# Kernel tuning notes

Hardware: AMD Instinct MI355X
Metric: run time of the kernel (lower is better)

The kernel has to match this reference:

```python
import jax, jax.numpy as jnp
import numpy as np

N, E, IN, H, OUT, L = 100000, 1600000, 128, 64, 64, 3


def setup_inputs() -> dict:
    key = jax.random.key(0)
    ks = jax.random.split(key, 20)
    g = lambda i, shape: jax.random.normal(ks[i], shape, dtype=jnp.float32) * 0.05
    # architecture mixture weights: softmax of log_alpha ~ N(1, 0.01)
    sm = lambda i, rows, n: jax.nn.softmax(1.0 + 0.01 * jax.random.normal(ks[i], (rows, n), dtype=jnp.float32), axis=-1)
    return dict(
        x=jax.random.normal(ks[0], (N, IN), dtype=jnp.float32),
        edge_index=jax.random.randint(ks[1], (2, E), 0, N, dtype=jnp.int32),
        W_pre=g(2, (IN, H)), b_pre=jnp.zeros((H,), jnp.float32),
        W_self=g(3, (L, H, H)), b_self=jnp.zeros((L, H), jnp.float32),
        W_nbr=g(4, (L, H, H)), b_nbr=jnp.zeros((L, H), jnp.float32),
        W_comb=g(5, (L, 2 * H, H)), b_comb=jnp.zeros((L, H), jnp.float32),
        W_lc=g(6, (L, 2 * H, H)), b_lc=jnp.zeros((L, H), jnp.float32),
        ln_g=jnp.ones((L, H), jnp.float32), ln_b=jnp.zeros((L, H), jnp.float32),
        prelu_w=jnp.full((L,), 0.25, jnp.float32),
        W_lagg=g(7, ((L + 1) * H, H)), b_lagg=jnp.zeros((H,), jnp.float32),
        W_ff1=g(8, (H, H)), b_ff1=jnp.zeros((H,), jnp.float32),
        W_ff2=g(9, (H, OUT)), b_ff2=jnp.zeros((OUT,), jnp.float32),
        Z_agg=sm(10, L, 3), Z_comb=sm(11, L, 2), Z_act=sm(12, L, 2),
        Z_lc=sm(13, L, 3), Z_lagg=sm(14, 1, 3),
    )


def _layernorm(x, g, b, eps=1e-5):
    mu = x.mean(-1, keepdims=True)
    var = ((x - mu) ** 2).mean(-1, keepdims=True)
    return (x - mu) / jnp.sqrt(var + eps) * g + b


def reference(x, edge_index, W_pre, b_pre, W_self, b_self, W_nbr, b_nbr,
              W_comb, b_comb, W_lc, b_lc, ln_g, ln_b, prelu_w,
              W_lagg, b_lagg, W_ff1, b_ff1, W_ff2, b_ff2,
              Z_agg, Z_comb, Z_act, Z_lc, Z_lagg):
    n = x.shape[0]
    src, tgt = edge_index[0], edge_index[1]
    cnt = jax.ops.segment_sum(jnp.ones((src.shape[0], 1), x.dtype), tgt, num_segments=n)
    x = x @ W_pre + b_pre                       # preprocess: [N, H]
    embs = [x]
    for i in range(L):
        x_self = x @ W_self[i] + b_self[i]
        x_nl = x @ W_nbr[i] + b_nbr[i]
        msg = x_nl[src]                         # gather messages [E, H]
        s = jax.ops.segment_sum(msg, tgt, num_segments=n)
        mean = s / jnp.maximum(cnt, 1.0)
        mx = jax.ops.segment_max(msg, tgt, num_segments=n)
        mx = jnp.where(cnt > 0, mx, 0.0)        # empty segments -> 0 (PyG convention)
        x_n = Z_agg[i, 0] * s + Z_agg[i, 1] * mean + Z_agg[i, 2] * mx
        # combine mixture: sum / concat+merge
        c_sum = x_self + x_n
        c_cat = jnp.concatenate([x_self, x_n], -1) @ W_comb[i] + b_comb[i]
        h = Z_comb[i, 0] * c_sum + Z_comb[i, 1] * c_cat
        # act mixture: relu / prelu
        h = Z_act[i, 0] * jax.nn.relu(h) + Z_act[i, 1] * jnp.where(h > 0, h, prelu_w[i] * h)
        h = _layernorm(h, ln_g[i], ln_b[i])
        embs.append(h)
        # layer_connect mixture: stack / skip_sum / skip_cat
        lc_cat = jnp.concatenate([embs[-2], embs[-1]], -1) @ W_lc[i] + b_lc[i]
        x = Z_lc[i, 0] * h + Z_lc[i, 1] * (h + embs[-2]) + Z_lc[i, 2] * lc_cat
    # layer_agg mixture: none / max_pooling / concat+merge over emb_list
    a_none = embs[-1]
    a_max = jnp.stack(embs, 0).max(0)
    a_cat = jnp.concatenate(embs, -1) @ W_lagg + b_lagg
    out = Z_lagg[0, 0] * a_none + Z_lagg[0, 1] * a_max + Z_lagg[0, 2] * a_cat
    # feed-forward head (node-level task, no global pooling)
    out = jax.nn.relu(out @ W_ff1 + b_ff1) @ W_ff2 + b_ff2
    return out
```

## Files before the change

### kernel.cpp

```cpp
#include <hip/hip_runtime.h>

typedef unsigned short u16;
typedef unsigned int u32;
using bfrag = __attribute__((ext_vector_type(8))) short;
using f4v   = __attribute__((ext_vector_type(4))) float;

#define DIV_UP(a,b) (((a)+(b)-1)/(b))
#define PTILE 4096
#define CHB 512
#define CHSH 9
#define NBKT 256
#define MFMA(a,b,c) __builtin_amdgcn_mfma_f32_16x16x32_bf16(a,b,c,0,0,0)

__device__ inline u16 f2bf(float f){
  union { float f; u32 u; } v; v.f = f;
  u32 u = v.u;
  return (u16)((u + 0x7fffu + ((u >> 16) & 1u)) >> 16);
}
__device__ inline float bf2f(u16 h){
  union { u32 u; float f; } v; v.u = ((u32)h) << 16;
  return v.f;
}
__device__ inline bfrag ldA(const u16* A, long r, int koff, int lane){
  return *reinterpret_cast<const bfrag*>(A + r*64 + koff + ((lane>>4)<<3));
}
__device__ inline bfrag ldW(const u16* Wf, int kb, int cb, int lane){
  return *reinterpret_cast<const bfrag*>(Wf + (((kb*4+cb)*64 + lane)<<3));
}

__device__ inline void xpose_store(u16* sT, int lane, const f4v (&acc)[4]){
  const int cl = lane & 15, g = lane >> 4;
#pragma unroll
  for (int j = 0; j < 4; ++j){
    const int lr = g*4 + j;
#pragma unroll
    for (int cb = 0; cb < 4; ++cb){
      const int colblk = cb*2 + (cl >> 3);
      const int gr = colblk ^ (lr & 7);
      sT[lr*64 + gr*8 + (cl & 7)] = f2bf(acc[cb][j]);
    }
  }
}
__device__ inline bfrag xpose_load(const u16* sT, int lane, int kb){
  const int row = lane & 15, colblk = kb*4 + (lane >> 4);
  const int gr = colblk ^ (row & 7);
  return *reinterpret_cast<const bfrag*>(sT + row*64 + gr*8);
}

__global__ void initBkt_k(int* __restrict__ bktCnt, int bstride){
  if (threadIdx.x < NBKT) bktCnt[threadIdx.x] = threadIdx.x * bstride;
}
__global__ void partition_k(const int* __restrict__ tgt, const int* __restrict__ src,
                            int E, int* __restrict__ bktCnt, int2* __restrict__ bkt){
  __shared__ int hist[NBKT], base[NBKT], pos[NBKT];
  const int t = threadIdx.x;
  hist[t] = 0;
  __syncthreads();
  const int e0 = blockIdx.x * PTILE;
  const int e1 = (e0 + PTILE < E) ? e0 + PTILE : E;
  for (int i = e0 + t; i < e1; i += NBKT)
    atomicAdd(&hist[tgt[i] >> CHSH], 1);
  __syncthreads();
  base[t] = (hist[t] > 0) ? atomicAdd(&bktCnt[t], hist[t]) : 0;
  pos[t] = 0;
  __syncthreads();
  for (int i = e0 + t; i < e1; i += NBKT){
    int tv = tgt[i], sv = src[i];
    int c = tv >> CHSH;
    int p = base[c] + atomicAdd(&pos[c], 1);
    bkt[p] = make_int2(tv, sv);
  }
}

__global__ __launch_bounds__(CHB) void sortChunk_k(const int2* __restrict__ bkt,
    const int* __restrict__ bktCnt, int bstride, int N,
    int* __restrict__ cnt, int* __restrict__ off, int* __restrict__ perm){
  __shared__ int hist[CHB], sbase[CHB];
  const int c = blockIdx.x, t = threadIdx.x;
  const int lo = c * CHB;
  const int s = c * bstride, e = bktCnt[c];
  hist[t] = 0;
  __syncthreads();
  for (int i = s + t; i < e; i += CHB)
    atomicAdd(&hist[bkt[i].x - lo], 1);
  __syncthreads();
  const int v = hist[t];
  for (int o = 1; o < CHB; o <<= 1){
    int add = (t >= o) ? hist[t - o] : 0;
    __syncthreads();
    hist[t] += add;
    __syncthreads();
  }
  const int excl = hist[t] - v;
  if (lo + t < N){ cnt[lo + t] = v; off[lo + t] = s + excl; }
  sbase[t] = s + excl;
  __syncthreads();
  hist[t] = 0;
  __syncthreads();
  for (int i = s + t; i < e; i += CHB){
    int2 ed = bkt[i];
    int r = ed.x - lo;
    int p = sbase[r] + atomicAdd(&hist[r], 1);
    perm[p] = ed.y;
  }
}

__global__ void matW_k(const float* __restrict__ W_self, const float* __restrict__ W_comb,
                       const float* __restrict__ b_self,
                       float* __restrict__ WsWct, float* __restrict__ bsWct){
  const int b = blockIdx.x;
  const int i = b / 65, r = b % 65;
  const int c = threadIdx.x;
  const float* Wc = W_comb + i*8192;
  float s = 0.f;
  if (r < 64){
    const float* a = W_self + i*4096 + r*64;
#pragma unroll 8
    for (int k = 0; k < 64; ++k) s += a[k] * Wc[k*64 + c];
    WsWct[i*4096 + r*64 + c] = s;
  } else {
    const float* a = b_self + i*64;
#pragma unroll 8
    for (int k = 0; k < 64; ++k) s += a[k] * Wc[k*64 + c];
    bsWct[i*64 + c] = s;
  }
}

__global__ void buildAll_k(const float* __restrict__ W_self, const float* __restrict__ W_comb,
    const float* __restrict__ b_self, const float* __restrict__ b_comb,
    const float* __restrict__ Z_comb, const float* __restrict__ WsWct,
    const float* __restrict__ bsWct,
    const float* __restrict__ W_lc, const float* __restrict__ b_lc,
    const float* __restrict__ Z_lc,
    const float* __restrict__ W_lagg, const float* __restrict__ b_lagg,
    const float* __restrict__ Z_lagg,
    float* __restrict__ W1eff, float* __restrict__ W2eff, float* __restrict__ beff,
    float* __restrict__ Wlceff, float* __restrict__ blceff,
    float* __restrict__ Wle, float* __restrict__ ble){
  int idx = blockIdx.x*blockDim.x + threadIdx.x;
  if (idx < 12288){
    int i = idx >> 12, rem = idx & 4095, k = rem >> 6, c = rem & 63;
    float zc0 = Z_comb[i*2], zc1 = Z_comb[i*2+1];
    W1eff[idx] = zc0*W_self[idx] + zc1*WsWct[idx];
    W2eff[idx] = (k == c ? zc0 : 0.f) + zc1*W_comb[i*8192 + (64 + k)*64 + c];
    return;
  }
  idx -= 12288;
  if (idx < 16384){
    int i = idx >> 13, rem = idx & 8191, k = rem >> 6, c = rem & 63;
    float z0 = Z_lc[i*3], z1 = Z_lc[i*3+1], z2 = Z_lc[i*3+2];
    float idv = (k < 64) ? (k == c ? z1 : 0.f) : ((k - 64) == c ? (z0 + z1) : 0.f);
    Wlceff[idx] = z2*W_lc[idx] + idv;
    return;
  }
  idx -= 16384;
  if (idx < 20480){
    int k = idx >> 6, c = idx & 63;
    float v = (k < 256) ? Z_lagg[2]*W_lagg[idx] : 0.f;
    if (k >= 192 && k < 256 && (k - 192) == c) v += Z_lagg[0];
    if (k >= 256 && (k - 256) == c) v += Z_lagg[1];
    Wle[idx] = v;
    return;
  }
  idx -= 20480;
  if (idx < 192){
    int i = idx >> 6;
    float zc0 = Z_comb[i*2], zc1 = Z_comb[i*2+1];
    beff[idx] = zc0*b_self[idx] + zc1*(bsWct[idx] + b_comb[idx]);
    return;
  }
  idx -= 192;
  if (idx < 128){
    int i = idx >> 6;
    blceff[idx] = Z_lc[i*3+2]*b_lc[idx];
    return;
  }
  idx -= 128;
  if (idx < 64) ble[idx] = Z_lagg[2]*b_lagg[idx];
}

struct PackJobs {
  const float* src[15];
  u16* dst[15];
  int nkb[15];
};
__global__ void pack_all_k(PackJobs pj){
  const int job = blockIdx.x >> 4, kb = blockIdx.x & 15;
  if (kb >= pj.nkb[job]) return;
  const int t = threadIdx.x, cb = t >> 6, lane = t & 63;
  const float* S = pj.src[job];
  u16* D = pj.dst[job] + (((kb*4 + cb)*64 + lane) << 3);
  const int kbase = kb*32 + ((lane >> 4) << 3), c = cb*16 + (lane & 15);
#pragma unroll
  for (int j = 0; j < 8; ++j) D[j] = f2bf(S[(kbase + j)*64 + c]);
}

__global__ __launch_bounds__(256) void gemmP_k(const float* __restrict__ X,
    const u16* __restrict__ Wf, const float* __restrict__ bias,
    const u16* __restrict__ Wn, const float* __restrict__ bn,
    u16* __restrict__ out, u16* __restrict__ xnl, int N){
  __shared__ u16 sT[4][1024];
  const int lane = threadIdx.x & 63, w = threadIdx.x >> 6;
  const int R = blockIdx.x*64 + w*16;
  bfrag wf[4][4], wn[2][4];
#pragma unroll
  for (int kb = 0; kb < 4; ++kb)
#pragma unroll
    for (int cb = 0; cb < 4; ++cb) wf[kb][cb] = ldW(Wf, kb, cb, lane);
#pragma unroll
  for (int kb = 0; kb < 2; ++kb)
#pragma unroll
    for (int cb = 0; cb < 4; ++cb) wn[kb][cb] = ldW(Wn, kb, cb, lane);
  float bv[4], bnv[4];
#pragma unroll
  for (int cb = 0; cb < 4; ++cb){ bv[cb] = bias[cb*16 + (lane & 15)]; bnv[cb] = bn[cb*16 + (lane & 15)]; }
  const long ra = (R + (lane & 15) < N) ? (R + (lane & 15)) : (N - 1);
  f4v acc[4] = {f4v{0,0,0,0}, f4v{0,0,0,0}, f4v{0,0,0,0}, f4v{0,0,0,0}};
#pragma unroll
  for (int kb = 0; kb < 4; ++kb){
    const float* ap = X + ra*128 + kb*32 + ((lane >> 4) << 3);
    float4 q0 = *reinterpret_cast<const float4*>(ap);
    float4 q1 = *reinterpret_cast<const float4*>(ap + 4);
    bfrag a;
    a[0] = (short)f2bf(q0.x); a[1] = (short)f2bf(q0.y);
    a[2] = (short)f2bf(q0.z); a[3] = (short)f2bf(q0.w);
    a[4] = (short)f2bf(q1.x); a[5] = (short)f2bf(q1.y);
    a[6] = (short)f2bf(q1.z); a[7] = (short)f2bf(q1.w);
#pragma unroll
    for (int cb = 0; cb < 4; ++cb) acc[cb] = MFMA(a, wf[kb][cb], acc[cb]);
  }
#pragma unroll
  for (int cb = 0; cb < 4; ++cb)
#pragma unroll
    for (int j = 0; j < 4; ++j) acc[cb][j] += bv[cb];
  const int rbase = R + ((lane >> 4) << 2), cl = lane & 15;
#pragma unroll
  for (int cb = 0; cb < 4; ++cb)
#pragma unroll
    for (int j = 0; j < 4; ++j){
      int r = rbase + j;
      if (r < N) out[(size_t)r*64 + cb*16 + cl] = f2bf(acc[cb][j]);
    }
  xpose_store(sT[w], lane, acc);
  f4v ac2[4] = {f4v{0,0,0,0}, f4v{0,0,0,0}, f4v{0,0,0,0}, f4v{0,0,0,0}};
#pragma unroll
  for (int kb = 0; kb < 2; ++kb){
    bfrag a = xpose_load(sT[w], lane, kb);
#pragma unroll
    for (int cb = 0; cb < 4; ++cb) ac2[cb] = MFMA(a, wn[kb][cb], ac2[cb]);
  }
#pragma unroll
  for (int cb = 0; cb < 4; ++cb)
#pragma unroll
    for (int j = 0; j < 4; ++j){
      int r = rbase + j;
      if (r < N) xnl[(size_t)r*64 + cb*16 + cl] = f2bf(ac2[cb][j] + bnv[cb]);
    }
}

__global__ __launch_bounds__(256) void gemmC_k(const u16* __restrict__ A1,
    const u16* __restrict__ A2, const u16* __restrict__ Wf1, const u16* __restrict__ Wf2,
    const float* __restrict__ beff, const float* __restrict__ lng, const float* __restrict__ lnb,
    const float* __restrict__ Zact, const float* __restrict__ prelu,
    u16* __restrict__ out, int N){
  const int lane = threadIdx.x & 63, w = threadIdx.x >> 6;
  const int R = blockIdx.x*64 + w*16;
  bfrag wf1[2][4], wf2[2][4];
#pragma unroll
  for (int kb = 0; kb < 2; ++kb)
#pragma unroll
    for (int cb = 0; cb < 4; ++cb){ wf1[kb][cb] = ldW(Wf1, kb, cb, lane); wf2[kb][cb] = ldW(Wf2, kb, cb, lane); }
  float bv[4], lgv[4], lbv[4];
#pragma unroll
  for (int cb = 0; cb < 4; ++cb){
    int c = cb*16 + (lane & 15);
    bv[cb] = beff[c]; lgv[cb] = lng[c]; lbv[cb] = lnb[c];
  }
  const float zt0 = Zact[0], zt1 = Zact[1], pw = prelu[0];
  const long ra = (R + (lane & 15) < N) ? (R + (lane & 15)) : (N - 1);
  f4v acc[4] = {f4v{0,0,0,0}, f4v{0,0,0,0}, f4v{0,0,0,0}, f4v{0,0,0,0}};
#pragma unroll
  for (int kb = 0; kb < 2; ++kb){
    bfrag a = ldA(A1, ra, kb*32, lane);
#pragma unroll
    for (int cb = 0; cb < 4; ++cb) acc[cb] = MFMA(a, wf1[kb][cb], acc[cb]);
  }
#pragma unroll
  for (int kb = 0; kb < 2; ++kb){
    bfrag a = ldA(A2, ra, kb*32, lane);
#pragma unroll
    for (int cb = 0; cb < 4; ++cb) acc[cb] = MFMA(a, wf2[kb][cb], acc[cb]);
  }
#pragma unroll
  for (int cb = 0; cb < 4; ++cb)
#pragma unroll
    for (int j = 0; j < 4; ++j){
      float v = acc[cb][j] + bv[cb];
      v = zt0*fmaxf(v, 0.f) + zt1*((v > 0.f) ? v : pw*v);
      acc[cb][j] = v;
    }
  const int rbase = R + ((lane >> 4) << 2), cl = lane & 15;
#pragma unroll
  for (int j = 0; j < 4; ++j){
    float s = acc[0][j] + acc[1][j] + acc[2][j] + acc[3][j];
    s += __shfl_xor(s, 1, 64); s += __shfl_xor(s, 2, 64);
    s += __shfl_xor(s, 4, 64); s += __shfl_xor(s, 8, 64);
    float mu = s * 0.015625f;
    float d0 = acc[0][j]-mu, d1 = acc[1][j]-mu, d2 = acc[2][j]-mu, d3 = acc[3][j]-mu;
    float q = d0*d0 + d1*d1 + d2*d2 + d3*d3;
    q += __shfl_xor(q, 1, 64); q += __shfl_xor(q, 2, 64);
    q += __shfl_xor(q, 4, 64); q += __shfl_xor(q, 8, 64);
    float sd = rsqrtf(q * 0.015625f + 1e-5f);
    int r = rbase + j;
    if (r < N){
      out[(size_t)r*64 +  0 + cl] = f2bf(d0*sd*lgv[0] + lbv[0]);
      out[(size_t)r*64 + 16 + cl] = f2bf(d1*sd*lgv[1] + lbv[1]);
      out[(size_t)r*64 + 32 + cl] = f2bf(d2*sd*lgv[2] + lbv[2]);
      out[(size_t)r*64 + 48 + cl] = f2bf(d3*sd*lgv[3] + lbv[3]);
    }
  }
}

__global__ __launch_bounds__(256) void gemmCL_k(const u16* __restrict__ A1,
    const u16* __restrict__ A2, const u16* __restrict__ Aprev,
    const u16* __restrict__ Wf1, const u16* __restrict__ Wf2,
    const float* __restrict__ beff, const float* __restrict__ lng, const float* __restrict__ lnb,
    const float* __restrict__ Zact, const float* __restrict__ prelu,
    const u16* __restrict__ Wlc, const float* __restrict__ blc,
    const u16* __restrict__ Wn, const float* __restrict__ bn,
    u16* __restrict__ emb_out, u16* __restrict__ x_out, u16* __restrict__ xnl, int N){
  __shared__ u16 sT[4][1024];
  const int lane = threadIdx.x & 63, w = threadIdx.x >> 6;
  const int R = blockIdx.x*64 + w*16;
  bfrag wf1[2][4], wf2[2][4];
#pragma unroll
  for (int kb = 0; kb < 2; ++kb)
#pragma unroll
    for (int cb = 0; cb < 4; ++cb){ wf1[kb][cb] = ldW(Wf1, kb, cb, lane); wf2[kb][cb] = ldW(Wf2, kb, cb, lane); }
  float bv[4], lgv[4], lbv[4], blcv[4], bnv[4];
#pragma unroll
  for (int cb = 0; cb < 4; ++cb){
    int c = cb*16 + (lane & 15);
    bv[cb] = beff[c]; lgv[cb] = lng[c]; lbv[cb] = lnb[c];
    blcv[cb] = blc[c]; bnv[cb] = bn[c];
  }
  const float zt0 = Zact[0], zt1 = Zact[1], pw = prelu[0];
  const long ra = (R + (lane & 15) < N) ? (R + (lane & 15)) : (N - 1);
  f4v acc[4] = {f4v{0,0,0,0}, f4v{0,0,0,0}, f4v{0,0,0,0}, f4v{0,0,0,0}};
#pragma unroll
  for (int kb = 0; kb < 2; ++kb){
    bfrag a = ldA(A1, ra, kb*32, lane);
#pragma unroll
    for (int cb = 0; cb < 4; ++cb) acc[cb] = MFMA(a, wf1[kb][cb], acc[cb]);
  }
#pragma unroll
  for (int kb = 0; kb < 2; ++kb){
    bfrag a = ldA(A2, ra, kb*32, lane);
#pragma unroll
    for (int cb = 0; cb < 4; ++cb) acc[cb] = MFMA(a, wf2[kb][cb], acc[cb]);
  }
#pragma unroll
  for (int cb = 0; cb < 4; ++cb)
#pragma unroll
    for (int j = 0; j < 4; ++j){
      float v = acc[cb][j] + bv[cb];
      v = zt0*fmaxf(v, 0.f) + zt1*((v > 0.f) ? v : pw*v);
      acc[cb][j] = v;
    }
  const int rbase = R + ((lane >> 4) << 2), cl = lane & 15;
#pragma unroll
  for (int j = 0; j < 4; ++j){
    float s = acc[0][j] + acc[1][j] + acc[2][j] + acc[3][j];
    s += __shfl_xor(s, 1, 64); s += __shfl_xor(s, 2, 64);
    s += __shfl_xor(s, 4, 64); s += __shfl_xor(s, 8, 64);
    float mu = s * 0.015625f;
    float d0 = acc[0][j]-mu, d1 = acc[1][j]-mu, d2 = acc[2][j]-mu, d3 = acc[3][j]-mu;
    float q = d0*d0 + d1*d1 + d2*d2 + d3*d3;
    q += __shfl_xor(q, 1, 64); q += __shfl_xor(q, 2, 64);
    q += __shfl_xor(q, 4, 64); q += __shfl_xor(q, 8, 64);
    float sd = rsqrtf(q * 0.015625f + 1e-5f);
    acc[0][j] = d0*sd*lgv[0] + lbv[0];
    acc[1][j] = d1*sd*lgv[1] + lbv[1];
    acc[2][j] = d2*sd*lgv[2] + lbv[2];
    acc[3][j] = d3*sd*lgv[3] + lbv[3];
    int r = rbase + j;
    if (r < N){
      emb_out[(size_t)r*64 +  0 + cl] = f2bf(acc[0][j]);
      emb_out[(size_t)r*64 + 16 + cl] = f2bf(acc[1][j]);
      emb_out[(size_t)r*64 + 32 + cl] = f2bf(acc[2][j]);
      emb_out[(size_t)r*64 + 48 + cl] = f2bf(acc[3][j]);
    }
  }
  xpose_store(sT[w], lane, acc);
  f4v ac2[4] = {f4v{0,0,0,0}, f4v{0,0,0,0}, f4v{0,0,0,0}, f4v{0,0,0,0}};
#pragma unroll
  for (int kb = 0; kb < 4; ++kb){
    bfrag a = (kb < 2) ? ldA(Aprev, ra, kb*32, lane) : xpose_load(sT[w], lane, kb - 2);
#pragma unroll
    for (int cb = 0; cb < 4; ++cb) ac2[cb] = MFMA(a, ldW(Wlc, kb, cb, lane), ac2[cb]);
  }
#pragma unroll
  for (int cb = 0; cb < 4; ++cb)
#pragma unroll
    for (int j = 0; j < 4; ++j) ac2[cb][j] += blcv[cb];
#pragma unroll
  for (int cb = 0; cb < 4; ++cb)
#pragma unroll
    for (int j = 0; j < 4; ++j){
      int r = rbase + j;
      if (r < N) x_out[(size_t)r*64 + cb*16 + cl] = f2bf(ac2[cb][j]);
    }
  xpose_store(sT[w], lane, ac2);
  f4v ac3[4] = {f4v{0,0,0,0}, f4v{0,0,0,0}, f4v{0,0,0,0}, f4v{0,0,0,0}};
#pragma unroll
  for (int kb = 0; kb < 2; ++kb){
    bfrag a = xpose_load(sT[w], lane, kb);
#pragma unroll
    for (int cb = 0; cb < 4; ++cb) ac3[cb] = MFMA(a, ldW(Wn, kb, cb, lane), ac3[cb]);
  }
#pragma unroll
  for (int cb = 0; cb < 4; ++cb)
#pragma unroll
    for (int j = 0; j < 4; ++j){
      int r = rbase + j;
      if (r < N) xnl[(size_t)r*64 + cb*16 + cl] = f2bf(ac3[cb][j] + bnv[cb]);
    }
}

__global__ __launch_bounds__(256) void gemmL_k(const u16* __restrict__ e0,
    const u16* __restrict__ e1, const u16* __restrict__ e2, const u16* __restrict__ e3,
    const u16* __restrict__ Wf, const float* __restrict__ bias,
    u16* __restrict__ out, int N){
  const int lane = threadIdx.x & 63, w = threadIdx.x >> 6;
  const int R = blockIdx.x*64 + w*16;
  const u16* Ab[4] = {e0, e1, e2, e3};
  float bv[4];
#pragma unroll
  for (int cb = 0; cb < 4; ++cb) bv[cb] = bias[cb*16 + (lane & 15)];
  const long ra = (R + (lane & 15) < N) ? (R + (lane & 15)) : (N - 1);
  f4v acc[4] = {f4v{0,0,0,0}, f4v{0,0,0,0}, f4v{0,0,0,0}, f4v{0,0,0,0}};
  bfrag mx[2];
#pragma unroll
  for (int kb = 0; kb < 8; ++kb){
    bfrag a = ldA(Ab[kb >> 1], ra, (kb & 1)*32, lane);
    if (kb < 2){ mx[kb] = a; }
    else {
      bfrag& m = mx[kb & 1];
#pragma unroll
      for (int i = 0; i < 8; ++i)
        m[i] = (short)f2bf(fmaxf(bf2f((u16)m[i]), bf2f((u16)a[i])));
    }
#pragma unroll
    for (int cb = 0; cb < 4; ++cb) acc[cb] = MFMA(a, ldW(Wf, kb, cb, lane), acc[cb]);
  }
#pragma unroll
  for (int kb = 8; kb < 10; ++kb)
#pragma unroll
    for (int cb = 0; cb < 4; ++cb) acc[cb] = MFMA(mx[kb-8], ldW(Wf, kb, cb, lane), acc[cb]);
  const int rbase = R + ((lane >> 4) << 2), cl = lane & 15;
#pragma unroll
  for (int cb = 0; cb < 4; ++cb)
#pragma unroll
    for (int j = 0; j < 4; ++j){
      int r = rbase + j;
      if (r < N) out[(size_t)r*64 + cb*16 + cl] = f2bf(acc[cb][j] + bv[cb]);
    }
}

__global__ __launch_bounds__(256) void ff12_k(const u16* __restrict__ A,
    const u16* __restrict__ Wf1, const float* __restrict__ b1,
    const u16* __restrict__ Wf2, const float* __restrict__ b2,
    float* __restrict__ out, int N){
  __shared__ u16 sT[4][1024];
  const int lane = threadIdx.x & 63, w = threadIdx.x >> 6;
  const int R = blockIdx.x*64 + w*16;
  bfrag wf1[2][4], wf2[2][4];
#pragma unroll
  for (int kb = 0; kb < 2; ++kb)
#pragma unroll
    for (int cb = 0; cb < 4; ++cb){ wf1[kb][cb] = ldW(Wf1, kb, cb, lane); wf2[kb][cb] = ldW(Wf2, kb, cb, lane); }
  float bv1[4], bv2[4];
#pragma unroll
  for (int cb = 0; cb < 4; ++cb){ bv1[cb] = b1[cb*16 + (lane & 15)]; bv2[cb] = b2[cb*16 + (lane & 15)]; }
  const long ra = (R + (lane & 15) < N) ? (R + (lane & 15)) : (N - 1);
  f4v acc[4] = {f4v{0,0,0,0}, f4v{0,0,0,0}, f4v{0,0,0,0}, f4v{0,0,0,0}};
#pragma unroll
  for (int kb = 0; kb < 2; ++kb){
    bfrag a = ldA(A, ra, kb*32, lane);
#pragma unroll
    for (int cb = 0; cb < 4; ++cb) acc[cb] = MFMA(a, wf1[kb][cb], acc[cb]);
  }
#pragma unroll
  for (int cb = 0; cb < 4; ++cb)
#pragma unroll
    for (int j = 0; j < 4; ++j) acc[cb][j] = fmaxf(acc[cb][j] + bv1[cb], 0.f);
  xpose_store(sT[w], lane, acc);
  f4v ac2[4] = {f4v{0,0,0,0}, f4v{0,0,0,0}, f4v{0,0,0,0}, f4v{0,0,0,0}};
#pragma unroll
  for (int kb = 0; kb < 2; ++kb){
    bfrag a = xpose_load(sT[w], lane, kb);
#pragma unroll
    for (int cb = 0; cb < 4; ++cb) ac2[cb] = MFMA(a, wf2[kb][cb], ac2[cb]);
  }
  const int rbase = R + ((lane >> 4) << 2), cl = lane & 15;
#pragma unroll
  for (int cb = 0; cb < 4; ++cb)
#pragma unroll
    for (int j = 0; j < 4; ++j){
      int r = rbase + j;
      if (r < N) out[(size_t)r*64 + cb*16 + cl] = ac2[cb][j] + bv2[cb];
    }
}

__global__ __launch_bounds__(256) void gather_k(const u16* __restrict__ xnl,
    const int* __restrict__ off, const int* __restrict__ cnt, const int* __restrict__ perm,
    const float* __restrict__ Z_agg, int layer, u16* __restrict__ xn, int N){
  const int lane = threadIdx.x & 63, w = threadIdx.x >> 6;
  const int g = lane >> 3;
  const int q = lane & 7;
  const int gbase = lane & 56;
  const int r = blockIdx.x*32 + w*8 + g;
  const float za0 = Z_agg[layer*3+0], za1 = Z_agg[layer*3+1], za2 = Z_agg[layer*3+2];
  int e0 = 0, deg = 0;
  if (r < N){ e0 = off[r]; deg = cnt[r]; }
  const float NI = -3.402823466e38f;
  float s0=0.f,s1=0.f,s2=0.f,s3=0.f,s4=0.f,s5=0.f,s6=0.f,s7=0.f;
  float m0=NI,m1=NI,m2=NI,m3=NI,m4=NI,m5=NI,m6=NI,m7=NI;
  const u16* xq = xnl + q*8;
  int pe = (q < deg) ? perm[e0 + q] : 0;
  for (int base = 0; base < deg; base += 8){
    int pe_n = (base + 8 + q < deg) ? perm[e0 + base + 8 + q] : 0;
    int idx[8];
#pragma unroll
    for (int j = 0; j < 8; ++j) idx[j] = __shfl(pe, gbase + j, 64);
    uint4 ub[8];
#pragma unroll
    for (int j = 0; j < 8; ++j)
      ub[j] = *reinterpret_cast<const uint4*>(xq + ((size_t)idx[j] << 6));
#pragma unroll
    for (int j = 0; j < 8; ++j){
      if (base + j < deg){
        uint4 u = ub[j];
        float a0 = __uint_as_float(u.x << 16), a1 = __uint_as_float(u.x & 0xffff0000u);
        float a2 = __uint_as_float(u.y << 16), a3 = __uint_as_float(u.y & 0xffff0000u);
        float a4 = __uint_as_float(u.z << 16), a5 = __uint_as_float(u.z & 0xffff0000u);
        float a6 = __uint_as_float(u.w << 16), a7 = __uint_as_float(u.w & 0xffff0000u);
        s0 += a0; s1 += a1; s2 += a2; s3 += a3;
        s4 += a4; s5 += a5; s6 += a6; s7 += a7;
        m0 = fmaxf(m0, a0); m1 = fmaxf(m1, a1); m2 = fmaxf(m2, a2); m3 = fmaxf(m3, a3);
        m4 = fmaxf(m4, a4); m5 = fmaxf(m5, a5); m6 = fmaxf(m6, a6); m7 = fmaxf(m7, a7);
      }
    }
    pe = pe_n;
  }
  if (r < N){
    const float inv = 1.f / fmaxf((float)deg, 1.f);
    const float gz = (deg > 0) ? 1.f : 0.f;
    const float ca = za0 + za1*inv, cm = za2*gz;
    uint4 o;
    o.x = (u32)f2bf(ca*s0 + cm*m0) | (((u32)f2bf(ca*s1 + cm*m1)) << 16);
    o.y = (u32)f2bf(ca*s2 + cm*m2) | (((u32)f2bf(ca*s3 + cm*m3)) << 16);
    o.z = (u32)f2bf(ca*s4 + cm*m4) | (((u32)f2bf(ca*s5 + cm*m5)) << 16);
    o.w = (u32)f2bf(ca*s6 + cm*m6) | (((u32)f2bf(ca*s7 + cm*m7)) << 16);
    reinterpret_cast<uint4*>(xn + ((size_t)r << 6))[q] = o;
  }
}

extern "C" void kernel_launch(void* const* d_in, const int* in_sizes, int n_in,
                              void* d_out, int out_size, void* d_ws, size_t ws_size,
                              hipStream_t stream){
  const float* x      = (const float*)d_in[0];
  const int*   ei     = (const int*)  d_in[1];
  const float* W_pre  = (const float*)d_in[2];
  const float* b_pre  = (const float*)d_in[3];
  const float* W_self = (const float*)d_in[4];
  const float* b_self = (const float*)d_in[5];
  const float* W_nbr  = (const float*)d_in[6];
  const float* b_nbr  = (const float*)d_in[7];
  const float* W_comb = (const float*)d_in[8];
  const float* b_comb = (const float*)d_in[9];
  const float* W_lc   = (const float*)d_in[10];
  const float* b_lc   = (const float*)d_in[11];
  const float* ln_g   = (const float*)d_in[12];
  const float* ln_b   = (const float*)d_in[13];
  const float* prelu  = (const float*)d_in[14];
  const float* W_lagg = (const float*)d_in[15];
  const float* b_lagg = (const float*)d_in[16];
  const float* W_ff1  = (const float*)d_in[17];
  const float* b_ff1  = (const float*)d_in[18];
  const float* W_ff2  = (const float*)d_in[19];
  const float* b_ff2  = (const float*)d_in[20];
  const float* Z_agg  = (const float*)d_in[21];
  const float* Z_comb = (const float*)d_in[22];
  const float* Z_act  = (const float*)d_in[23];
  const float* Z_lc   = (const float*)d_in[24];
  const float* Z_lagg = (const float*)d_in[25];

  const int N = in_sizes[0] / 128;
  const int E = in_sizes[1] / 2;
  const int* src = ei;
  const int* tgt = ei + E;

  const int nch = DIV_UP(N, CHB);
  const int bstride = (int)(((long)E * CHB) / N) + 2048;

  char* p = (char*)d_ws;
  auto carve = [&](size_t bytes)->void*{
    void* q = (void*)p;
    p += (bytes + 255) & ~(size_t)255;
    return q;
  };
  int* cnt_i = (int*)carve((size_t)N*4);
  int* off   = (int*)carve((size_t)N*4);
  int* bktCnt= (int*)carve(NBKT*4);
  int2* bkt  = (int2*)carve((size_t)NBKT*bstride*8);
  int* perm  = (int*)carve((size_t)NBKT*bstride*4);
  float* WsWct = (float*)carve(3*4096*4);
  float* bsWct = (float*)carve(3*64*4);
  float* W1eff = (float*)carve(3*4096*4);
  float* W2eff = (float*)carve(3*4096*4);
  float* beff  = (float*)carve(3*64*4);
  float* Wlceff= (float*)carve(2*8192*4);
  float* blceff= (float*)carve(2*64*4);
  float* Wle   = (float*)carve(20480*4);
  float* ble   = (float*)carve(64*4);
  u16* pWpre = (u16*)carve(8192*2);
  u16* pWnbr = (u16*)carve(3*4096*2);
  u16* pW1   = (u16*)carve(3*4096*2);
  u16* pW2   = (u16*)carve(3*4096*2);
  u16* pWlc  = (u16*)carve(2*8192*2);
  u16* pWlagg= (u16*)carve(20480*2);
  u16* pWff1 = (u16*)carve(4096*2);
  u16* pWff2 = (u16*)carve(4096*2);
  const size_t AB = (size_t)N*64*2;
  u16* emb0 = (u16*)carve(AB);
  u16* emb1 = (u16*)carve(AB);
  u16* emb2 = (u16*)carve(AB);
  u16* emb3 = (u16*)carve(AB);
  u16* xbuf = (u16*)carve(AB);
  u16* xnl  = (u16*)carve(AB);
  u16* xn   = (u16*)carve(AB);
  u16* mixb = (u16*)carve(AB);

  initBkt_k<<<1,NBKT,0,stream>>>(bktCnt, bstride);
  partition_k<<<DIV_UP(E,PTILE),NBKT,0,stream>>>(tgt, src, E, bktCnt, bkt);
  sortChunk_k<<<nch,CHB,0,stream>>>(bkt, bktCnt, bstride, N, cnt_i, off, perm);

  matW_k<<<3*65,64,0,stream>>>(W_self, W_comb, b_self, WsWct, bsWct);
  buildAll_k<<<DIV_UP(49536,256),256,0,stream>>>(W_self, W_comb, b_self, b_comb, Z_comb,
                                                 WsWct, bsWct, W_lc, b_lc, Z_lc,
                                                 W_lagg, b_lagg, Z_lagg,
                                                 W1eff, W2eff, beff, Wlceff, blceff, Wle, ble);

  PackJobs pj;
  pj.src[0] = W_pre;  pj.dst[0] = pWpre;  pj.nkb[0] = 4;
  for (int i = 0; i < 3; ++i){
    pj.src[1+i] = W_nbr + i*4096; pj.dst[1+i] = pWnbr + i*4096; pj.nkb[1+i] = 2;
    pj.src[4+i] = W1eff + i*4096; pj.dst[4+i] = pW1   + i*4096; pj.nkb[4+i] = 2;
    pj.src[7+i] = W2eff + i*4096; pj.dst[7+i] = pW2   + i*4096; pj.nkb[7+i] = 2;
  }
  pj.src[10] = Wlceff;        pj.dst[10] = pWlc;        pj.nkb[10] = 4;
  pj.src[11] = Wlceff + 8192; pj.dst[11] = pWlc + 8192; pj.nkb[11] = 4;
  pj.src[12] = Wle;   pj.dst[12] = pWlagg; pj.nkb[12] = 10;
  pj.src[13] = W_ff1; pj.dst[13] = pWff1;  pj.nkb[13] = 2;
  pj.src[14] = W_ff2; pj.dst[14] = pWff2;  pj.nkb[14] = 2;
  pack_all_k<<<15*16,256,0,stream>>>(pj);

  const int G64 = DIV_UP(N, 64);

  gemmP_k<<<G64,256,0,stream>>>(x, pWpre, b_pre, pWnbr, b_nbr, emb0, xnl, N);

  u16* embs[4] = {emb0, emb1, emb2, emb3};
  const u16* xin = emb0;
  for (int i = 0; i < 3; ++i){
    gather_k<<<DIV_UP(N,32),256,0,stream>>>(xnl, off, cnt_i, perm, Z_agg, i, xn, N);
    if (i < 2){
      gemmCL_k<<<G64,256,0,stream>>>(xin, xn, embs[i],
                                     pW1 + i*4096, pW2 + i*4096,
                                     beff + i*64, ln_g + i*64, ln_b + i*64,
                                     Z_act + i*2, prelu + i,
                                     pWlc + i*8192, blceff + i*64,
                                     pWnbr + (i+1)*4096, b_nbr + (i+1)*64,
                                     embs[i+1], xbuf, xnl, N);
      xin = xbuf;
    } else {
      gemmC_k<<<G64,256,0,stream>>>(xin, xn, pW1 + i*4096, pW2 + i*4096,
                                    beff + i*64, ln_g + i*64, ln_b + i*64,
                                    Z_act + i*2, prelu + i, embs[i+1], N);
    }
  }

  gemmL_k<<<G64,256,0,stream>>>(emb0, emb1, emb2, emb3, pWlagg, ble, mixb, N);
  ff12_k<<<G64,256,0,stream>>>(mixb, pWff1, b_ff1, pWff2, b_ff2, (float*)d_out, N);
}
```

Before: 268.5 us.

## Fuse layer-agg and FF head, pack bucket edges, stage partition in LDS, double-buffer gather

Merges the layer-aggregation GEMM and the two-layer feed-forward head into one kernel, so the intermediate mix buffer is never written to or read back from global memory. Packs each bucketed edge into a single 32-bit word (local target in the high bits, source in the low 17 bits), which halves bucket traffic but assumes N fits in 17 bits. The partition kernel now stages tgt/src tiles in shared memory with vectorized loads instead of reading them twice from global. The gather loop is double-buffered so the next batch of neighbour loads is in flight while the current one is reduced, at the cost of more registers.

```diff
diff --git a/kernel.cpp b/kernel.cpp
--- a/kernel.cpp
+++ b/kernel.cpp
@@ -51,28 +51,37 @@
   if (threadIdx.x < NBKT) bktCnt[threadIdx.x] = threadIdx.x * bstride;
 }
 __global__ void partition_k(const int* __restrict__ tgt, const int* __restrict__ src,
-                            int E, int* __restrict__ bktCnt, int2* __restrict__ bkt){
+                            int E, int* __restrict__ bktCnt, u32* __restrict__ bkt){
+  __shared__ int sTgt[PTILE], sSrc[PTILE];
   __shared__ int hist[NBKT], base[NBKT], pos[NBKT];
   const int t = threadIdx.x;
+  const int e0 = blockIdx.x * PTILE;
+  const int n = (e0 + PTILE < E) ? PTILE : (E - e0);
+  const int n4 = n >> 2;
+  for (int i = t; i < n4; i += NBKT){
+    reinterpret_cast<int4*>(sTgt)[i] = reinterpret_cast<const int4*>(tgt + e0)[i];
+    reinterpret_cast<int4*>(sSrc)[i] = reinterpret_cast<const int4*>(src + e0)[i];
+  }
+  for (int i = (n4 << 2) + t; i < n; i += NBKT){
+    sTgt[i] = tgt[e0 + i]; sSrc[i] = src[e0 + i];
+  }
   hist[t] = 0;
   __syncthreads();
-  const int e0 = blockIdx.x * PTILE;
-  const int e1 = (e0 + PTILE < E) ? e0 + PTILE : E;
-  for (int i = e0 + t; i < e1; i += NBKT)
-    atomicAdd(&hist[tgt[i] >> CHSH], 1);
+  for (int i = t; i < n; i += NBKT)
+    atomicAdd(&hist[sTgt[i] >> CHSH], 1);
   __syncthreads();
   base[t] = (hist[t] > 0) ? atomicAdd(&bktCnt[t], hist[t]) : 0;
   pos[t] = 0;
   __syncthreads();
-  for (int i = e0 + t; i < e1; i += NBKT){
-    int tv = tgt[i], sv = src[i];
+  for (int i = t; i < n; i += NBKT){
+    int tv = sTgt[i], sv = sSrc[i];
     int c = tv >> CHSH;
     int p = base[c] + atomicAdd(&pos[c], 1);
-    bkt[p] = make_int2(tv, sv);
-  }
-}
-
-__global__ __launch_bounds__(CHB) void sortChunk_k(const int2* __restrict__ bkt,
+    bkt[p] = ((u32)(tv & (CHB - 1)) << 17) | (u32)sv;
+  }
+}
+
+__global__ __launch_bounds__(CHB) void sortChunk_k(const u32* __restrict__ bkt,
     const int* __restrict__ bktCnt, int bstride, int N,
     int* __restrict__ cnt, int* __restrict__ off, int* __restrict__ perm){
   __shared__ int hist[CHB], sbase[CHB];
@@ -82,7 +91,7 @@
   hist[t] = 0;
   __syncthreads();
   for (int i = s + t; i < e; i += CHB)
-    atomicAdd(&hist[bkt[i].x - lo], 1);
+    atomicAdd(&hist[bkt[i] >> 17], 1);
   __syncthreads();
   const int v = hist[t];
   for (int o = 1; o < CHB; o <<= 1){
@@ -98,10 +107,10 @@
   hist[t] = 0;
   __syncthreads();
   for (int i = s + t; i < e; i += CHB){
-    int2 ed = bkt[i];
-    int r = ed.x - lo;
+    u32 ed = bkt[i];
+    int r = (int)(ed >> 17);
     int p = sbase[r] + atomicAdd(&hist[r], 1);
-    perm[p] = ed.y;
+    perm[p] = (int)(ed & 0x1FFFFu);
   }
 }
 
@@ -427,80 +436,65 @@
     }
 }
 
-__global__ __launch_bounds__(256) void gemmL_k(const u16* __restrict__ e0,
+__global__ __launch_bounds__(256) void gemmLF_k(const u16* __restrict__ e0,
     const u16* __restrict__ e1, const u16* __restrict__ e2, const u16* __restrict__ e3,
     const u16* __restrict__ Wf, const float* __restrict__ bias,
-    u16* __restrict__ out, int N){
-  const int lane = threadIdx.x & 63, w = threadIdx.x >> 6;
-  const int R = blockIdx.x*64 + w*16;
-  const u16* Ab[4] = {e0, e1, e2, e3};
-  float bv[4];
-#pragma unroll
-  for (int cb = 0; cb < 4; ++cb) bv[cb] = bias[cb*16 + (lane & 15)];
-  const long ra = (R + (lane & 15) < N) ? (R + (lane & 15)) : (N - 1);
-  f4v acc[4] = {f4v{0,0,0,0}, f4v{0,0,0,0}, f4v{0,0,0,0}, f4v{0,0,0,0}};
-  bfrag mx[2];
-#pragma unroll
-  for (int kb = 0; kb < 8; ++kb){
-    bfrag a = ldA(Ab[kb >> 1], ra, (kb & 1)*32, lane);
-    if (kb < 2){ mx[kb] = a; }
-    else {
-      bfrag& m = mx[kb & 1];
-#pragma unroll
-      for (int i = 0; i < 8; ++i)
-        m[i] = (short)f2bf(fmaxf(bf2f((u16)m[i]), bf2f((u16)a[i])));
-    }
-#pragma unroll
-    for (int cb = 0; cb < 4; ++cb) acc[cb] = MFMA(a, ldW(Wf, kb, cb, lane), acc[cb]);
-  }
-#pragma unroll
-  for (int kb = 8; kb < 10; ++kb)
-#pragma unroll
-    for (int cb = 0; cb < 4; ++cb) acc[cb] = MFMA(mx[kb-8], ldW(Wf, kb, cb, lane), acc[cb]);
-  const int rbase = R + ((lane >> 4) << 2), cl = lane & 15;
-#pragma unroll
-  for (int cb = 0; cb < 4; ++cb)
-#pragma unroll
-    for (int j = 0; j < 4; ++j){
-      int r = rbase + j;
-      if (r < N) out[(size_t)r*64 + cb*16 + cl] = f2bf(acc[cb][j] + bv[cb]);
-    }
-}
-
-__global__ __launch_bounds__(256) void ff12_k(const u16* __restrict__ A,
     const u16* __restrict__ Wf1, const float* __restrict__ b1,
     const u16* __restrict__ Wf2, const float* __restrict__ b2,
     float* __restrict__ out, int N){
   __shared__ u16 sT[4][1024];
   const int lane = threadIdx.x & 63, w = threadIdx.x >> 6;
   const int R = blockIdx.x*64 + w*16;
-  bfrag wf1[2][4], wf2[2][4];
-#pragma unroll
-  for (int kb = 0; kb < 2; ++kb)
-#pragma unroll
-    for (int cb = 0; cb < 4; ++cb){ wf1[kb][cb] = ldW(Wf1, kb, cb, lane); wf2[kb][cb] = ldW(Wf2, kb, cb, lane); }
-  float bv1[4], bv2[4];
-#pragma unroll
-  for (int cb = 0; cb < 4; ++cb){ bv1[cb] = b1[cb*16 + (lane & 15)]; bv2[cb] = b2[cb*16 + (lane & 15)]; }
+  const u16* Ab[4] = {e0, e1, e2, e3};
+  float bv[4], bv1[4], bv2[4];
+#pragma unroll
+  for (int cb = 0; cb < 4; ++cb){
+    int c = cb*16 + (lane & 15);
+    bv[cb] = bias[c]; bv1[cb] = b1[c]; bv2[cb] = b2[c];
+  }
   const long ra = (R + (lane & 15) < N) ? (R + (lane & 15)) : (N - 1);
   f4v acc[4] = {f4v{0,0,0,0}, f4v{0,0,0,0}, f4v{0,0,0,0}, f4v{0,0,0,0}};
-#pragma unroll
-  for (int kb = 0; kb < 2; ++kb){
-    bfrag a = ldA(A, ra, kb*32, lane);
-#pragma unroll
-    for (int cb = 0; cb < 4; ++cb) acc[cb] = MFMA(a, wf1[kb][cb], acc[cb]);
-  }
-#pragma unroll
-  for (int cb = 0; cb < 4; ++cb)
-#pragma unroll
-    for (int j = 0; j < 4; ++j) acc[cb][j] = fmaxf(acc[cb][j] + bv1[cb], 0.f);
+  bfrag mx[2];
+#pragma unroll
+  for (int kb = 0; kb < 8; ++kb){
+    bfrag a = ldA(Ab[kb >> 1], ra, (kb & 1)*32, lane);
+    if (kb < 2){ mx[kb] = a; }
+    else {
+      bfrag& m = mx[kb & 1];
+#pragma unroll
+      for (int i = 0; i < 8; ++i)
+        m[i] = (short)f2bf(fmaxf(bf2f((u16)m[i]), bf2f((u16)a[i])));
+    }
+#pragma unroll
+    for (int cb = 0; cb < 4; ++cb) acc[cb] = MFMA(a, ldW(Wf, kb, cb, lane), acc[cb]);
+  }
+#pragma unroll
+  for (int kb = 8; kb < 10; ++kb)
+#pragma unroll
+    for (int cb = 0; cb < 4; ++cb) acc[cb] = MFMA(mx[kb-8], ldW(Wf, kb, cb, lane), acc[cb]);
+#pragma unroll
+  for (int cb = 0; cb < 4; ++cb)
+#pragma unroll
+    for (int j = 0; j < 4; ++j) acc[cb][j] += bv[cb];
   xpose_store(sT[w], lane, acc);
   f4v ac2[4] = {f4v{0,0,0,0}, f4v{0,0,0,0}, f4v{0,0,0,0}, f4v{0,0,0,0}};
 #pragma unroll
   for (int kb = 0; kb < 2; ++kb){
     bfrag a = xpose_load(sT[w], lane, kb);
 #pragma unroll
-    for (int cb = 0; cb < 4; ++cb) ac2[cb] = MFMA(a, wf2[kb][cb], ac2[cb]);
+    for (int cb = 0; cb < 4; ++cb) ac2[cb] = MFMA(a, ldW(Wf1, kb, cb, lane), ac2[cb]);
+  }
+#pragma unroll
+  for (int cb = 0; cb < 4; ++cb)
+#pragma unroll
+    for (int j = 0; j < 4; ++j) ac2[cb][j] = fmaxf(ac2[cb][j] + bv1[cb], 0.f);
+  xpose_store(sT[w], lane, ac2);
+  f4v ac3[4] = {f4v{0,0,0,0}, f4v{0,0,0,0}, f4v{0,0,0,0}, f4v{0,0,0,0}};
+#pragma unroll
+  for (int kb = 0; kb < 2; ++kb){
+    bfrag a = xpose_load(sT[w], lane, kb);
+#pragma unroll
+    for (int cb = 0; cb < 4; ++cb) ac3[cb] = MFMA(a, ldW(Wf2, kb, cb, lane), ac3[cb]);
   }
   const int rbase = R + ((lane >> 4) << 2), cl = lane & 15;
 #pragma unroll
@@ -508,7 +502,7 @@
 #pragma unroll
     for (int j = 0; j < 4; ++j){
       int r = rbase + j;
-      if (r < N) out[(size_t)r*64 + cb*16 + cl] = ac2[cb][j] + bv2[cb];
+      if (r < N) out[(size_t)r*64 + cb*16 + cl] = ac3[cb][j] + bv2[cb];
     }
 }
 
@@ -524,44 +518,67 @@
   int e0 = 0, deg = 0;
   if (r < N){ e0 = off[r]; deg = cnt[r]; }
   const float NI = -3.402823466e38f;
-  float s0=0.f,s1=0.f,s2=0.f,s3=0.f,s4=0.f,s5=0.f,s6=0.f,s7=0.f;
-  float m0=NI,m1=NI,m2=NI,m3=NI,m4=NI,m5=NI,m6=NI,m7=NI;
+  float s[8], m[8];
+#pragma unroll
+  for (int k = 0; k < 8; ++k){ s[k] = 0.f; m[k] = NI; }
   const u16* xq = xnl + q*8;
-  int pe = (q < deg) ? perm[e0 + q] : 0;
-  for (int base = 0; base < deg; base += 8){
-    int pe_n = (base + 8 + q < deg) ? perm[e0 + base + 8 + q] : 0;
-    int idx[8];
-#pragma unroll
-    for (int j = 0; j < 8; ++j) idx[j] = __shfl(pe, gbase + j, 64);
-    uint4 ub[8];
-#pragma unroll
-    for (int j = 0; j < 8; ++j)
-      ub[j] = *reinterpret_cast<const uint4*>(xq + ((size_t)idx[j] << 6));
+  auto consume = [&](const uint4 (&ub)[8], int base){
 #pragma unroll
     for (int j = 0; j < 8; ++j){
       if (base + j < deg){
-        uint4 u = ub[j];
+        const uint4 u = ub[j];
         float a0 = __uint_as_float(u.x << 16), a1 = __uint_as_float(u.x & 0xffff0000u);
         float a2 = __uint_as_float(u.y << 16), a3 = __uint_as_float(u.y & 0xffff0000u);
         float a4 = __uint_as_float(u.z << 16), a5 = __uint_as_float(u.z & 0xffff0000u);
         float a6 = __uint_as_float(u.w << 16), a7 = __uint_as_float(u.w & 0xffff0000u);
-        s0 += a0; s1 += a1; s2 += a2; s3 += a3;
-        s4 += a4; s5 += a5; s6 += a6; s7 += a7;
-        m0 = fmaxf(m0, a0); m1 = fmaxf(m1, a1); m2 = fmaxf(m2, a2); m3 = fmaxf(m3, a3);
-        m4 = fmaxf(m4, a4); m5 = fmaxf(m5, a5); m6 = fmaxf(m6, a6); m7 = fmaxf(m7, a7);
+        s[0] += a0; s[1] += a1; s[2] += a2; s[3] += a3;
+        s[4] += a4; s[5] += a5; s[6] += a6; s[7] += a7;
+        m[0] = fmaxf(m[0], a0); m[1] = fmaxf(m[1], a1);
+        m[2] = fmaxf(m[2], a2); m[3] = fmaxf(m[3], a3);
+        m[4] = fmaxf(m[4], a4); m[5] = fmaxf(m[5], a5);
+        m[6] = fmaxf(m[6], a6); m[7] = fmaxf(m[7], a7);
       }
     }
-    pe = pe_n;
+  };
+  int idxA[8]; uint4 ubA[8];
+  int idxB[8]; uint4 ubB[8];
+  {
+    int pe = (q < deg) ? perm[e0 + q] : 0;
+#pragma unroll
+    for (int j = 0; j < 8; ++j) idxA[j] = __shfl(pe, gbase + j, 64);
+#pragma unroll
+    for (int j = 0; j < 8; ++j)
+      ubA[j] = *reinterpret_cast<const uint4*>(xq + ((size_t)idxA[j] << 6));
+  }
+  for (int base = 0; base < deg; base += 16){
+    {
+      int pe = (base + 8 + q < deg) ? perm[e0 + base + 8 + q] : 0;
+#pragma unroll
+      for (int j = 0; j < 8; ++j) idxB[j] = __shfl(pe, gbase + j, 64);
+#pragma unroll
+      for (int j = 0; j < 8; ++j)
+        ubB[j] = *reinterpret_cast<const uint4*>(xq + ((size_t)idxB[j] << 6));
+    }
+    consume(ubA, base);
+    {
+      int pe = (base + 16 + q < deg) ? perm[e0 + base + 16 + q] : 0;
+#pragma unroll
+      for (int j = 0; j < 8; ++j) idxA[j] = __shfl(pe, gbase + j, 64);
+#pragma unroll
+      for (int j = 0; j < 8; ++j)
+        ubA[j] = *reinterpret_cast<const uint4*>(xq + ((size_t)idxA[j] << 6));
+    }
+    consume(ubB, base + 8);
   }
   if (r < N){
     const float inv = 1.f / fmaxf((float)deg, 1.f);
     const float gz = (deg > 0) ? 1.f : 0.f;
     const float ca = za0 + za1*inv, cm = za2*gz;
     uint4 o;
-    o.x = (u32)f2bf(ca*s0 + cm*m0) | (((u32)f2bf(ca*s1 + cm*m1)) << 16);
-    o.y = (u32)f2bf(ca*s2 + cm*m2) | (((u32)f2bf(ca*s3 + cm*m3)) << 16);
-    o.z = (u32)f2bf(ca*s4 + cm*m4) | (((u32)f2bf(ca*s5 + cm*m5)) << 16);
-    o.w = (u32)f2bf(ca*s6 + cm*m6) | (((u32)f2bf(ca*s7 + cm*m7)) << 16);
+    o.x = (u32)f2bf(ca*s[0] + cm*m[0]) | (((u32)f2bf(ca*s[1] + cm*m[1])) << 16);
+    o.y = (u32)f2bf(ca*s[2] + cm*m[2]) | (((u32)f2bf(ca*s[3] + cm*m[3])) << 16);
+    o.z = (u32)f2bf(ca*s[4] + cm*m[4]) | (((u32)f2bf(ca*s[5] + cm*m[5])) << 16);
+    o.w = (u32)f2bf(ca*s[6] + cm*m[6]) | (((u32)f2bf(ca*s[7] + cm*m[7])) << 16);
     reinterpret_cast<uint4*>(xn + ((size_t)r << 6))[q] = o;
   }
 }
@@ -613,7 +630,7 @@
   int* cnt_i = (int*)carve((size_t)N*4);
   int* off   = (int*)carve((size_t)N*4);
   int* bktCnt= (int*)carve(NBKT*4);
-  int2* bkt  = (int2*)carve((size_t)NBKT*bstride*8);
+  u32* bkt   = (u32*)carve((size_t)NBKT*bstride*4);
   int* perm  = (int*)carve((size_t)NBKT*bstride*4);
   float* WsWct = (float*)carve(3*4096*4);
   float* bsWct = (float*)carve(3*64*4);
@@ -640,7 +657,6 @@
   u16* xbuf = (u16*)carve(AB);
   u16* xnl  = (u16*)carve(AB);
   u16* xn   = (u16*)carve(AB);
-  u16* mixb = (u16*)carve(AB);
 
   initBkt_k<<<1,NBKT,0,stream>>>(bktCnt, bstride);
   partition_k<<<DIV_UP(E,PTILE),NBKT,0,stream>>>(tgt, src, E, bktCnt, bkt);
@@ -690,6 +706,6 @@
     }
   }
 
-  gemmL_k<<<G64,256,0,stream>>>(emb0, emb1, emb2, emb3, pWlagg, ble, mixb, N);
-  ff12_k<<<G64,256,0,stream>>>(mixb, pWff1, b_ff1, pWff2, b_ff2, (float*)d_out, N);
-}
+  gemmLF_k<<<G64,256,0,stream>>>(emb0, emb1, emb2, emb3, pWlagg, ble,
+                                 pWff1, b_ff1, pWff2, b_ff2, (float*)d_out, N);
+}
```

Measured after the change: 257.7 us. -4.0%, faster.
